# Kernel optimization log

Measured on AMD Instinct MI355X. Metric: run time of the kernel, lower is better.

Reference implementation:

```python
import jax, jax.numpy as jnp
import numpy as np


def setup_inputs() -> dict:
    key = jax.random.key(0)
    k1, k2 = jax.random.split(key)
    B, C, H, W = 8, 64, 64, 64
    x = jax.random.normal(k1, (B, C, H, W), dtype=jnp.float32)
    stdv = 1.0 / np.sqrt(C)
    weight = jax.random.uniform(k2, (C, C), dtype=jnp.float32, minval=-stdv, maxval=stdv)
    return {"x": x, "weight": weight}


def reference(x, weight):
    B, C, H, W = x.shape
    N = H * W
    xf = x.reshape(B, C, N)            # [B, C, N]
    g_x = jnp.transpose(xf, (0, 2, 1))  # [B, N, C] (also theta_x)
    # f[b, i, j] = sum_c x[b, c, i] * x[b, c, j]
    f = jnp.einsum('bic,bcj->bij', g_x, xf)  # [B, N, N]
    adj = jax.nn.softmax(f, axis=-1)
    support = jnp.einsum('bnc,cd->bnd', g_x, weight)  # [B, N, C]
    y = jnp.einsum('bij,bjc->bic', adj, support)      # [B, N, C]
    y = jnp.transpose(y, (0, 2, 1)).reshape(B, C, H, W)
    return y + x
```

## Files before the change

### kernel.cpp

```cpp
#include <hip/hip_runtime.h>
#include <stdint.h>


#define NTOK 4096
#define CCH  64

typedef float v4f __attribute__((ext_vector_type(4)));
typedef __bf16 v8bf __attribute__((ext_vector_type(8)));
typedef unsigned short v8us __attribute__((ext_vector_type(8)));

__device__ __forceinline__ unsigned short f2bf(float f) {
    union { float f; unsigned int u; } c; c.f = f;
    unsigned int r = c.u + 0x7fffu + ((c.u >> 16) & 1u);
    return (unsigned short)(r >> 16);
}

__device__ __forceinline__ v8bf ld8(const unsigned short* p) {
    union { v8us s; v8bf b; } u;
    u.s = *(const v8us*)p;
    return u.b;
}

__device__ __forceinline__ unsigned int pkbf(float a, float b) {
    union { float f; unsigned int u; } ua, ub; ua.f = a; ub.f = b;
    return __builtin_amdgcn_perm(ub.u, ua.u, 0x07060302u);
}

__device__ __forceinline__ void gload_lds16(const void* g, void* l) {
    __builtin_amdgcn_global_load_lds(
        (const __attribute__((address_space(1))) unsigned int*)g,
        (__attribute__((address_space(3))) unsigned int*)l,
        16, 0, 0);
}

__global__ __launch_bounds__(256) void prep_kernel(
    const float* __restrict__ x,
    const float* __restrict__ w,
    unsigned short* __restrict__ xT,
    unsigned short* __restrict__ sT)
{
    __shared__ float Xf[64 * 65];

    const int tid  = threadIdx.x;
    const int lane = tid & 63;
    const int wv   = __builtin_amdgcn_readfirstlane(tid >> 6);
    const int b    = blockIdx.y;
    const int n0   = blockIdx.x * 64;

    const float* xb = x + (size_t)b * CCH * NTOK + n0 + lane;
    #pragma unroll
    for (int k = 0; k < 16; ++k) {
        const int c = wv * 16 + k;
        Xf[c * 65 + lane] = xb[(size_t)c * NTOK];
    }
    __syncthreads();

    {
        const int n  = tid >> 2;
        const int c0 = (tid & 3) * 16;
        unsigned int pk[8];
        #pragma unroll
        for (int k = 0; k < 8; ++k) {
            const float a = Xf[(c0 + 2 * k) * 65 + n];
            const float c2 = Xf[(c0 + 2 * k + 1) * 65 + n];
            pk[k] = (unsigned int)f2bf(a) | ((unsigned int)f2bf(c2) << 16);
        }
        unsigned short* xtr = xT + ((size_t)b * NTOK + n0 + n) * CCH + c0;
        *(uint4*)(xtr)     = *(uint4*)(pk);
        *(uint4*)(xtr + 8) = *(uint4*)(pk + 4);
    }

    float acc[16];
    #pragma unroll
    for (int d = 0; d < 16; ++d) acc[d] = 0.f;

    #pragma unroll 4
    for (int c = 0; c < 64; ++c) {
        const float xc = Xf[c * 65 + lane];
        const float* wr = w + c * 64 + wv * 16;
        #pragma unroll
        for (int d = 0; d < 16; ++d) acc[d] = fmaf(xc, wr[d], acc[d]);
    }
    unsigned short* stb = sT + (size_t)b * CCH * NTOK + n0 + lane;
    #pragma unroll
    for (int d = 0; d < 16; ++d)
        stb[(size_t)(wv * 16 + d) * NTOK] = f2bf(acc[d]);
}

__global__ __launch_bounds__(256, 4) void flash_kernel(
    const unsigned short* __restrict__ xT,
    const unsigned short* __restrict__ sT,
    float* __restrict__ part_o,
    float* __restrict__ part_l,
    int nchunk, int chunk_len)
{
    __shared__ __align__(16) unsigned short Kt[64 * 64];
    __shared__ __align__(16) unsigned short Vt[64 * 64];
    __shared__ __align__(16) unsigned short Pt[4][32 * 64];

    const int tid  = threadIdx.x;
    const int w    = tid >> 6;
    const int lane = tid & 63;
    const int quad = lane >> 4;
    const int l16  = lane & 15;
    const int l7   = l16 & 7;
    const int b     = blockIdx.z;
    const int chunk = blockIdx.y;
    const int i0   = blockIdx.x * 128;
    const int irow = i0 + w * 32;
    const int jb   = chunk * chunk_len;

    const unsigned short* xTb = xT + (size_t)b * NTOK * CCH;
    const unsigned short* sTb = sT + (size_t)b * CCH * NTOK;

    const int srow = w * 8 + (lane >> 3);
    const int sc   = (lane & 7) ^ (lane >> 3);
    unsigned short* kd0 = Kt + w * 512;
    unsigned short* vd0 = Vt + w * 512;

    v8bf aq0[2], aq1[2];
    #pragma unroll
    for (int m = 0; m < 2; ++m) {
        const unsigned short* qr = xTb + (size_t)(irow + m * 16 + l16) * CCH + quad * 8;
        aq0[m] = ld8(qr);
        aq1[m] = ld8(qr + 32);
    }

    float negm[2];
    #pragma unroll
    for (int m = 0; m < 2; ++m) {
        float msq = 0.f;
        #pragma unroll
        for (int i = 0; i < 8; ++i) {
            float e0 = (float)aq0[m][i], e1 = (float)aq1[m][i];
            msq = fmaf(e0, e0, msq);
            msq = fmaf(e1, e1, msq);
        }
        msq += __shfl_xor(msq, 16);
        msq += __shfl_xor(msq, 32);
        negm[m] = -msq;
    }

    v4f o[2][4];
    #pragma unroll
    for (int m = 0; m < 2; ++m)
        #pragma unroll
        for (int ct = 0; ct < 4; ++ct) { o[m][ct][0]=0.f; o[m][ct][1]=0.f; o[m][ct][2]=0.f; o[m][ct][3]=0.f; }
    float rsum[2] = {0.f, 0.f};

    unsigned short* Pw = Pt[w];
    const int phalf = (quad & 1) * 4;
    const int pgq   = quad >> 1;

    for (int jj = 0; jj < chunk_len; jj += 64) {
        const int j0 = jb + jj;

        gload_lds16(xTb + (size_t)(j0 + srow) * CCH + sc * 8,       kd0);
        gload_lds16(xTb + (size_t)(j0 + 32 + srow) * CCH + sc * 8,  kd0 + 2048);
        gload_lds16(sTb + (size_t)srow * NTOK + j0 + sc * 8,        vd0);
        gload_lds16(sTb + (size_t)(32 + srow) * NTOK + j0 + sc * 8, vd0 + 2048);
        __syncthreads();

        #pragma unroll
        for (int jt = 0; jt < 4; ++jt) {
            const int krow = 16 * jt + l16;
            const unsigned short* kb = Kt + krow * 64;
            const int c0 = quad ^ (krow & 7);
            v8bf bk0 = ld8(kb + c0 * 8);
            v8bf bk1 = ld8(kb + (c0 ^ 4) * 8);
            #pragma unroll
            for (int m = 0; m < 2; ++m) {
                v4f z; z[0]=0.f; z[1]=0.f; z[2]=0.f; z[3]=0.f;
                z = __builtin_amdgcn_mfma_f32_16x16x32_bf16(bk0, aq0[m], z, 0, 0, 0);
                z = __builtin_amdgcn_mfma_f32_16x16x32_bf16(bk1, aq1[m], z, 0, 0, 0);
                const float p0 = __expf(z[0] + negm[m]);
                const float p1 = __expf(z[1] + negm[m]);
                const float p2 = __expf(z[2] + negm[m]);
                const float p3 = __expf(z[3] + negm[m]);
                rsum[m] += (p0 + p1) + (p2 + p3);
                uint2 pk; pk.x = pkbf(p0, p1); pk.y = pkbf(p2, p3);
                const int pos = (2 * jt + pgq) ^ l7;
                *(uint2*)(Pw + (m * 16 + l16) * 64 + pos * 8 + phalf) = pk;
            }
        }

        v8bf pb0[2], pb1[2];
        #pragma unroll
        for (int m = 0; m < 2; ++m) {
            const unsigned short* pr = Pw + (m * 16 + l16) * 64;
            const int p0c = quad ^ l7;
            pb0[m] = ld8(pr + p0c * 8);
            pb1[m] = ld8(pr + (p0c ^ 4) * 8);
        }

        #pragma unroll
        for (int ct = 0; ct < 4; ++ct) {
            const int vrow = 16 * ct + l16;
            const unsigned short* vb = Vt + vrow * 64;
            const int c0 = quad ^ (vrow & 7);
            v8bf bv0 = ld8(vb + c0 * 8);
            v8bf bv1 = ld8(vb + (c0 ^ 4) * 8);
            #pragma unroll
            for (int m = 0; m < 2; ++m) {
                o[m][ct] = __builtin_amdgcn_mfma_f32_16x16x32_bf16(bv0, pb0[m], o[m][ct], 0, 0, 0);
                o[m][ct] = __builtin_amdgcn_mfma_f32_16x16x32_bf16(bv1, pb1[m], o[m][ct], 0, 0, 0);
            }
        }
        __syncthreads();
    }

    const size_t pbase = (size_t)(b * nchunk + chunk) * NTOK + irow;
    #pragma unroll
    for (int m = 0; m < 2; ++m) {
        float t = rsum[m];
        t += __shfl_xor(t, 16);
        t += __shfl_xor(t, 32);
        if (quad == 0) part_l[pbase + m * 16 + l16] = t;
    }
    float* po = part_o + pbase * 64;
    #pragma unroll
    for (int m = 0; m < 2; ++m)
        #pragma unroll
        for (int ct = 0; ct < 4; ++ct)
            *(v4f*)(po + (size_t)(m * 16 + l16) * 64 + ct * 16 + quad * 4) = o[m][ct];
}

__global__ __launch_bounds__(256, 2) void combine_kernel(
    const float* __restrict__ part_o,
    const float* __restrict__ part_l,
    const float* __restrict__ x,
    float* __restrict__ out,
    int nchunk)
{
    __shared__ float Of[64 * 65];
    const int tid = threadIdx.x;
    const int b = blockIdx.y;
    const int i0 = blockIdx.x * 64;
    const int row = tid >> 2;
    const int seg = tid & 3;

    float acc[16];
    #pragma unroll
    for (int k = 0; k < 16; ++k) acc[k] = 0.f;
    float lt = 0.f;

    for (int ch = 0; ch < nchunk; ++ch) {
        const size_t base = (size_t)(b * nchunk + ch) * NTOK + i0 + row;
        lt += part_l[base];
        const float* po = part_o + base * 64 + seg * 16;
        #pragma unroll
        for (int k = 0; k < 4; ++k) {
            float4 v = *(const float4*)(po + k * 4);
            acc[k*4+0] += v.x; acc[k*4+1] += v.y; acc[k*4+2] += v.z; acc[k*4+3] += v.w;
        }
    }
    const float inv = 1.f / lt;
    #pragma unroll
    for (int k = 0; k < 16; ++k) Of[row * 65 + seg * 16 + k] = acc[k] * inv;
    __syncthreads();

    const int c    = tid >> 2;
    const int part = tid & 3;
    const float* xrow = x   + ((size_t)b * CCH + c) * NTOK + i0 + part * 16;
    float*       orow = out + ((size_t)b * CCH + c) * NTOK + i0 + part * 16;
    #pragma unroll
    for (int i4 = 0; i4 < 4; ++i4) {
        float4 xv = *(const float4*)(xrow + i4 * 4);
        float4 ov;
        ov.x = Of[(part * 16 + i4 * 4 + 0) * 65 + c] + xv.x;
        ov.y = Of[(part * 16 + i4 * 4 + 1) * 65 + c] + xv.y;
        ov.z = Of[(part * 16 + i4 * 4 + 2) * 65 + c] + xv.z;
        ov.w = Of[(part * 16 + i4 * 4 + 3) * 65 + c] + xv.w;
        *(float4*)(orow + i4 * 4) = ov;
    }
}

extern "C" void kernel_launch(void* const* d_in, const int* in_sizes, int n_in,
                              void* d_out, int out_size, void* d_ws, size_t ws_size,
                              hipStream_t stream) {
    const float* x = (const float*)d_in[0];
    const float* w = (const float*)d_in[1];
    float* out = (float*)d_out;

    const size_t xT_elems = (size_t)8 * NTOK * CCH;
    unsigned short* xT = (unsigned short*)d_ws;
    unsigned short* sT = xT + xT_elems;
    char* rest = (char*)d_ws + 2 * xT_elems * sizeof(unsigned short);

    int KS = 4;
    while (KS > 1) {
        size_t need = 2 * xT_elems * sizeof(unsigned short)
                    + (size_t)KS * ((size_t)8 * NTOK * CCH * 4 + (size_t)8 * NTOK * 4);
        if (need <= ws_size) break;
        KS >>= 1;
    }
    float* part_o = (float*)rest;
    float* part_l = (float*)(rest + (size_t)KS * 8 * NTOK * CCH * 4);

    dim3 gp(64, 8);
    prep_kernel<<<gp, 256, 0, stream>>>(x, w, xT, sT);
    dim3 gf(32, KS, 8);
    flash_kernel<<<gf, 256, 0, stream>>>(xT, sT, part_o, part_l, KS, NTOK / KS);
    dim3 gc(64, 8);
    combine_kernel<<<gc, 256, 0, stream>>>(part_o, part_l, x, out, KS);
}
```

Measured before the change: 126.9 us.

## Double-buffer K/V tiles in LDS and use exp2 with folded log2e

The flash kernel now stages the next 64-token K/V tile into a second LDS buffer while the current tile is being computed. This leaves one barrier per iteration instead of two and is meant to hide global-to-LDS load latency. The softmax exponent becomes a hardware exp2 on an fma that scales by log2(e) with a prescaled offset. The extra LDS (48KB per block) drops the occupancy target from 4 to 3 blocks per CU, which may offset some of the latency-hiding benefit.

```diff
diff --git a/kernel.cpp b/kernel.cpp
--- a/kernel.cpp
+++ b/kernel.cpp
@@ -24,6 +24,14 @@
 __device__ __forceinline__ unsigned int pkbf(float a, float b) {
     union { float f; unsigned int u; } ua, ub; ua.f = a; ub.f = b;
     return __builtin_amdgcn_perm(ub.u, ua.u, 0x07060302u);
+}
+
+__device__ __forceinline__ float ex2(float x) {
+#if __has_builtin(__builtin_amdgcn_exp2f)
+    return __builtin_amdgcn_exp2f(x);
+#else
+    return exp2f(x);
+#endif
 }
 
 __device__ __forceinline__ void gload_lds16(const void* g, void* l) {
@@ -87,15 +95,15 @@
         stb[(size_t)(wv * 16 + d) * NTOK] = f2bf(acc[d]);
 }
 
-__global__ __launch_bounds__(256, 4) void flash_kernel(
+__global__ __launch_bounds__(256, 3) void flash_kernel(
     const unsigned short* __restrict__ xT,
     const unsigned short* __restrict__ sT,
     float* __restrict__ part_o,
     float* __restrict__ part_l,
     int nchunk, int chunk_len)
 {
-    __shared__ __align__(16) unsigned short Kt[64 * 64];
-    __shared__ __align__(16) unsigned short Vt[64 * 64];
+    __shared__ __align__(16) unsigned short Kt[2][64 * 64];
+    __shared__ __align__(16) unsigned short Vt[2][64 * 64];
     __shared__ __align__(16) unsigned short Pt[4][32 * 64];
 
     const int tid  = threadIdx.x;
@@ -115,8 +123,17 @@
 
     const int srow = w * 8 + (lane >> 3);
     const int sc   = (lane & 7) ^ (lane >> 3);
-    unsigned short* kd0 = Kt + w * 512;
-    unsigned short* vd0 = Vt + w * 512;
+
+    auto stage = [&](int j0, int bf) {
+        unsigned short* kd = Kt[bf] + w * 512;
+        unsigned short* vd = Vt[bf] + w * 512;
+        gload_lds16(xTb + (size_t)(j0 + srow) * CCH + sc * 8,       kd);
+        gload_lds16(xTb + (size_t)(j0 + 32 + srow) * CCH + sc * 8,  kd + 2048);
+        gload_lds16(sTb + (size_t)srow * NTOK + j0 + sc * 8,        vd);
+        gload_lds16(sTb + (size_t)(32 + srow) * NTOK + j0 + sc * 8, vd + 2048);
+    };
+
+    stage(jb, 0);
 
     v8bf aq0[2], aq1[2];
     #pragma unroll
@@ -126,7 +143,8 @@
         aq1[m] = ld8(qr + 32);
     }
 
-    float negm[2];
+    const float L2E = 1.4426950408889634f;
+    float negm2[2];
     #pragma unroll
     for (int m = 0; m < 2; ++m) {
         float msq = 0.f;
@@ -138,7 +156,7 @@
         }
         msq += __shfl_xor(msq, 16);
         msq += __shfl_xor(msq, 32);
-        negm[m] = -msq;
+        negm2[m] = -msq * L2E;
     }
 
     v4f o[2][4];
@@ -152,19 +170,19 @@
     const int phalf = (quad & 1) * 4;
     const int pgq   = quad >> 1;
 
+    int cur = 0;
     for (int jj = 0; jj < chunk_len; jj += 64) {
-        const int j0 = jb + jj;
-
-        gload_lds16(xTb + (size_t)(j0 + srow) * CCH + sc * 8,       kd0);
-        gload_lds16(xTb + (size_t)(j0 + 32 + srow) * CCH + sc * 8,  kd0 + 2048);
-        gload_lds16(sTb + (size_t)srow * NTOK + j0 + sc * 8,        vd0);
-        gload_lds16(sTb + (size_t)(32 + srow) * NTOK + j0 + sc * 8, vd0 + 2048);
         __syncthreads();
+        if (jj + 64 < chunk_len)
+            stage(jb + jj + 64, cur ^ 1);
+
+        const unsigned short* Kc = Kt[cur];
+        const unsigned short* Vc = Vt[cur];
 
         #pragma unroll
         for (int jt = 0; jt < 4; ++jt) {
             const int krow = 16 * jt + l16;
-            const unsigned short* kb = Kt + krow * 64;
+            const unsigned short* kb = Kc + krow * 64;
             const int c0 = quad ^ (krow & 7);
             v8bf bk0 = ld8(kb + c0 * 8);
             v8bf bk1 = ld8(kb + (c0 ^ 4) * 8);
@@ -173,10 +191,10 @@
                 v4f z; z[0]=0.f; z[1]=0.f; z[2]=0.f; z[3]=0.f;
                 z = __builtin_amdgcn_mfma_f32_16x16x32_bf16(bk0, aq0[m], z, 0, 0, 0);
                 z = __builtin_amdgcn_mfma_f32_16x16x32_bf16(bk1, aq1[m], z, 0, 0, 0);
-                const float p0 = __expf(z[0] + negm[m]);
-                const float p1 = __expf(z[1] + negm[m]);
-                const float p2 = __expf(z[2] + negm[m]);
-                const float p3 = __expf(z[3] + negm[m]);
+                const float p0 = ex2(fmaf(z[0], L2E, negm2[m]));
+                const float p1 = ex2(fmaf(z[1], L2E, negm2[m]));
+                const float p2 = ex2(fmaf(z[2], L2E, negm2[m]));
+                const float p3 = ex2(fmaf(z[3], L2E, negm2[m]));
                 rsum[m] += (p0 + p1) + (p2 + p3);
                 uint2 pk; pk.x = pkbf(p0, p1); pk.y = pkbf(p2, p3);
                 const int pos = (2 * jt + pgq) ^ l7;
@@ -196,7 +214,7 @@
         #pragma unroll
         for (int ct = 0; ct < 4; ++ct) {
             const int vrow = 16 * ct + l16;
-            const unsigned short* vb = Vt + vrow * 64;
+            const unsigned short* vb = Vc + vrow * 64;
             const int c0 = quad ^ (vrow & 7);
             v8bf bv0 = ld8(vb + c0 * 8);
             v8bf bv1 = ld8(vb + (c0 ^ 4) * 8);
@@ -206,7 +224,7 @@
                 o[m][ct] = __builtin_amdgcn_mfma_f32_16x16x32_bf16(bv1, pb1[m], o[m][ct], 0, 0, 0);
             }
         }
-        __syncthreads();
+        cur ^= 1;
     }
 
     const size_t pbase = (size_t)(b * nchunk + chunk) * NTOK + irow;
```

New measurement: 130.9 us. 1.03x slower.
